# Kernel tuning notes

Measured on AMD Instinct MI355X. Metric: run time of the kernel, lower is better.

Reference implementation:

```python
import jax, jax.numpy as jnp
import numpy as np

B, N, K, IN = 8, 2048, 8, 5
BN = B * N

def _lin(k, i, o):
    s = 1.0 / np.sqrt(i)
    return jax.random.uniform(k, (i, o), jnp.float32, -s, s)

def setup_inputs() -> dict:
    key = jax.random.key(0)
    ks = jax.random.split(key, 12)
    inp = {"points": jax.random.normal(ks[0], (B, N, IN), jnp.float32)}
    dims = [(IN * 2, 64), (64 * 2, 128), (128 * 2, 256)]
    for n, (i, o) in enumerate(dims, 1):
        inp[f"W{n}"] = _lin(ks[n], i, o)
        inp[f"b{n}"] = jnp.zeros((o,), jnp.float32)
        inp[f"g{n}"] = jnp.ones((o,), jnp.float32)
        inp[f"be{n}"] = jnp.zeros((o,), jnp.float32)
    inp["Wf1"] = _lin(ks[10], 448, 512); inp["bf1"] = jnp.zeros((512,), jnp.float32)
    inp["gf"] = jnp.ones((512,), jnp.float32); inp["bef"] = jnp.zeros((512,), jnp.float32)
    inp["Wf2"] = _lin(ks[11], 512, 128); inp["bf2"] = jnp.zeros((128,), jnp.float32)
    return inp

def _lrelu(x):
    return jnp.where(x >= 0, x, 0.2 * x)

def _bn(x, g, b, eps=1e-5):
    # BatchNorm1d in training mode: per-feature batch statistics
    m = x.mean(0)
    v = x.var(0)
    return (x - m) * jax.lax.rsqrt(v + eps) * g + b

def _knn_idx(pos):
    # pos: [B,N,3] -> neighbor indices [B,N,K], self excluded
    sq = (pos * pos).sum(-1)
    d = sq[:, :, None] + sq[:, None, :] - 2.0 * jnp.einsum('bnc,bmc->bnm', pos, pos)
    d = d + jnp.eye(N, dtype=d.dtype) * 1e10  # exclude self
    _, idx = jax.lax.top_k(-d, K)
    return idx

def _edge_conv(x, src, dst, W, b, g, be):
    # PyG EdgeConv: msg = nn(cat[x_i, x_j - x_i]); aggr='max' at target i
    xc = x[dst]
    xn = x[src]
    h = jnp.concatenate([xc, xn - xc], axis=-1) @ W + b
    h = _bn(_lrelu(h), g, be)
    return jax.ops.segment_max(h, dst, num_segments=BN)

def reference(points, W1, b1, g1, be1, W2, b2, g2, be2, W3, b3, g3, be3,
              Wf1, bf1, gf, bef, Wf2, bf2):
    pos = points[..., :3]                      # [B,N,3]
    idx = _knn_idx(pos)                        # [B,N,K]
    offs = (jnp.arange(B) * N)[:, None, None]
    src = (idx + offs).reshape(-1)             # neighbor (source) node ids [E]
    dst = jnp.repeat(jnp.arange(BN), K)        # center (target) node ids [E]
    x = points.reshape(BN, IN)
    x1 = _edge_conv(x, src, dst, W1, b1, g1, be1)   # [BN,64]
    x2 = _edge_conv(x1, src, dst, W2, b2, g2, be2)  # [BN,128]
    x3 = _edge_conv(x2, src, dst, W3, b3, g3, be3)  # [BN,256]
    xs = jnp.concatenate([x1, x2, x3], axis=-1).reshape(B, N, 448)
    gfeat = xs.max(axis=1)                     # global max pool per cloud [B,448]
    h = _bn(_lrelu(gfeat @ Wf1 + bf1), gf, bef)
    return h @ Wf2 + bf2                       # [B,128]
```

## Files before the change

kernel.cpp:

```cpp
#include <hip/hip_runtime.h>
#include <math.h>

#define B_ 8
#define N_ 2048
#define K_ 8
#define IN_ 5
#define BN_ (B_*N_)
#define NEDGE_ (BN_*K_)
#define GRP 8
#define SEG_ 32
#define CSEG_ (N_/SEG_)
#define CHUNKS_ (N_/GRP)

typedef unsigned short ushort8_ __attribute__((ext_vector_type(8)));
typedef short bf16x8_ __attribute__((ext_vector_type(8)));
typedef float f32x4_ __attribute__((ext_vector_type(4)));

__device__ inline unsigned short f2bf(float f) {
    unsigned int u = __float_as_uint(f);
    u += 0x7fffu + ((u >> 16) & 1u);
    return (unsigned short)(u >> 16);
}
__device__ inline float bf2f(unsigned short h) {
    return __uint_as_float(((unsigned int)h) << 16);
}

__device__ inline unsigned int ord_f32(float f) {
    unsigned int u = __float_as_uint(f);
    return (u & 0x80000000u) ? ~u : (u | 0x80000000u);
}

__global__ __launch_bounds__(256) void knn_part(const float4* __restrict__ P4,
                                                unsigned long long* __restrict__ part) {
    int tid = threadIdx.x;
    int q = blockIdx.x * 256 + tid;
    int b = q >> 11;
    int nloc = q & (N_-1);
    int seg = blockIdx.y;

    float4 qp = P4[q];
    float qx2 = -2.0f*qp.x, qy2 = -2.0f*qp.y, qz2 = -2.0f*qp.z;
    float qsq = qp.w;

    unsigned long long best[K_];
#pragma unroll
    for (int k = 0; k < K_; ++k) best[k] = ~0ull;

    const float4* __restrict__ cb = P4 + (size_t)b*N_ + (size_t)seg*CSEG_;
    int jbase = seg * CSEG_;

#pragma unroll 4
    for (int jj = 0; jj < CSEG_; ++jj) {
        float4 c = cb[jj];
        float d = qsq + c.w;
        d = fmaf(qx2, c.x, d);
        d = fmaf(qy2, c.y, d);
        d = fmaf(qz2, c.z, d);
        int jg = jbase + jj;
        d = (jg == nloc) ? INFINITY : d;
        unsigned long long cur = ((unsigned long long)ord_f32(d) << 32) | (unsigned int)jg;
#pragma unroll
        for (int p = 0; p < K_; ++p) {
            unsigned long long lo = best[p] < cur ? best[p] : cur;
            unsigned long long hi = best[p] < cur ? cur : best[p];
            best[p] = lo; cur = hi;
        }
    }
    unsigned long long* op = part + ((size_t)seg * BN_ + q) * K_;
#pragma unroll
    for (int k = 0; k < K_; ++k) op[k] = best[k];
}

__global__ __launch_bounds__(128) void knn_merge(const unsigned long long* __restrict__ part,
                                                 int* __restrict__ src) {
    int q = blockIdx.x * 128 + threadIdx.x;
    int b = q / N_;
    unsigned long long best[K_];
#pragma unroll
    for (int k = 0; k < K_; ++k) best[k] = ~0ull;
    for (int s = 0; s < SEG_; ++s) {
        const unsigned long long* lp = part + ((size_t)s * BN_ + q) * K_;
#pragma unroll
        for (int k = 0; k < K_; ++k) {
            unsigned long long key = lp[k];
            if (key >= best[K_-1]) break;
            unsigned long long cur = key;
#pragma unroll
            for (int p = 0; p < K_; ++p) {
                unsigned long long lo = best[p] < cur ? best[p] : cur;
                unsigned long long hi = best[p] < cur ? cur : best[p];
                best[p] = lo; cur = hi;
            }
        }
    }
#pragma unroll
    for (int k = 0; k < K_; ++k)
        src[(size_t)q*K_ + k] = b*N_ + (int)(best[k] & 0xFFFFFFFFu);
}

__global__ __launch_bounds__(256) void cast_split(const float* __restrict__ X,
                                                  unsigned short* __restrict__ Xh,
                                                  unsigned short* __restrict__ Xl,
                                                  float4* __restrict__ P4,
                                                  int Kin, int Kpad, int total8) {
    int t = blockIdx.x * 256 + threadIdx.x;
    if (t < total8) {
        int vpr = Kpad >> 3;
        int m = t / vpr;
        int k0 = (t % vpr) * 8;
        ushort8_ vh, vl;
#pragma unroll
        for (int j = 0; j < 8; ++j) {
            int k = k0 + j;
            float v = (k < Kin) ? X[(size_t)m*Kin + k] : 0.0f;
            unsigned short h = f2bf(v);
            vh[j] = h;
            vl[j] = f2bf(v - bf2f(h));
        }
        *(ushort8_*)(Xh + (size_t)m*Kpad + k0) = vh;
        *(ushort8_*)(Xl + (size_t)m*Kpad + k0) = vl;
    }
    if (t < BN_) {
        const float* p = X + (size_t)t*Kin;
        float x = p[0], y = p[1], z = p[2];
        P4[t] = make_float4(x, y, z, x*x + y*y + z*z);
    }
}

__global__ __launch_bounds__(256) void prep_layer(const float* __restrict__ W,
                                                  const float* __restrict__ scale,
                                                  const float* __restrict__ shift,
                                                  const float* __restrict__ bias,
                                                  unsigned short* __restrict__ WTh,
                                                  unsigned short* __restrict__ WTl,
                                                  float* __restrict__ cvec,
                                                  int Cin, int C, int Kpad) {
    int idx = blockIdx.x * 256 + threadIdx.x;
    int nWT = 2*C*Kpad;
    if (idx < nWT) {
        int n = idx / Kpad;
        int k = idx % Kpad;
        float val = 0.0f;
        if (k < Cin) {
            float s = scale ? scale[k] : 1.0f;
            if (n < C) val = s * (W[(size_t)k*C + n] - W[(size_t)(Cin+k)*C + n]);
            else       val = s * W[(size_t)(Cin+k)*C + (n - C)];
        }
        unsigned short h = f2bf(val);
        WTh[(size_t)n*Kpad + k] = h;
        WTl[(size_t)n*Kpad + k] = f2bf(val - bf2f(h));
    } else if (idx < nWT + C) {
        int c = idx - nWT;
        float acc = bias[c];
        if (shift)
            for (int d = 0; d < Cin; ++d) acc += shift[d] * W[(size_t)d*C + c];
        cvec[c] = acc;
    }
}

__global__ __launch_bounds__(256) void mfma_dual(const unsigned short* __restrict__ Xh,
                                                 const unsigned short* __restrict__ Xl,
                                                 const unsigned short* __restrict__ WTh,
                                                 const unsigned short* __restrict__ WTl,
                                                 float* __restrict__ PQ, int K, int Ntot,
                                                 int gx) {
    __shared__ unsigned short sXh[128*32], sXl[128*32], sWh[128*32], sWl[128*32];
    int n = blockIdx.x;
    int by = (n & 7) + 8*(n/(8*gx));
    int bx = (n >> 3) % gx;
    int tid = threadIdx.x, l = tid & 63, w = tid >> 6;
    int wr = w >> 1, wc = w & 1;
    int bm = by * 128, bn0 = bx * 128;

    f32x4_ acc[4][4];
#pragma unroll
    for (int i = 0; i < 4; ++i)
#pragma unroll
        for (int j = 0; j < 4; ++j) acc[i][j] = (f32x4_){0.f, 0.f, 0.f, 0.f};

    for (int k0 = 0; k0 < K; k0 += 32) {
#pragma unroll
        for (int i = 0; i < 2; ++i) {
            int idx = tid + i*256;
            int row = idx >> 2;
            int col0 = (idx & 3) * 8;
            size_t gxo = (size_t)(bm  + row)*K + k0 + col0;
            size_t gwo = (size_t)(bn0 + row)*K + k0 + col0;
            int lo_ = ((row << 6) | (col0 << 1)) ^ ((row & 7) << 4);
            *(ushort8_*)((char*)sXh + lo_) = *(const ushort8_*)(Xh + gxo);
            *(ushort8_*)((char*)sXl + lo_) = *(const ushort8_*)(Xl + gxo);
            *(ushort8_*)((char*)sWh + lo_) = *(const ushort8_*)(WTh + gwo);
            *(ushort8_*)((char*)sWl + lo_) = *(const ushort8_*)(WTl + gwo);
        }
        __syncthreads();

        int kb = (l >> 4) << 4;
        bf16x8_ bh[4], bl4[4];
#pragma unroll
        for (int nf = 0; nf < 4; ++nf) {
            int rn = wc*64 + nf*16 + (l & 15);
            int o = ((rn << 6) | kb) ^ ((rn & 7) << 4);
            bh[nf]  = *(const bf16x8_*)((const char*)sWh + o);
            bl4[nf] = *(const bf16x8_*)((const char*)sWl + o);
        }
#pragma unroll
        for (int mf = 0; mf < 4; ++mf) {
            int rm = wr*64 + mf*16 + (l & 15);
            int o = ((rm << 6) | kb) ^ ((rm & 7) << 4);
            bf16x8_ ah = *(const bf16x8_*)((const char*)sXh + o);
            bf16x8_ al = *(const bf16x8_*)((const char*)sXl + o);
#pragma unroll
            for (int nf = 0; nf < 4; ++nf) {
                acc[mf][nf] = __builtin_amdgcn_mfma_f32_16x16x32_bf16(ah, bh[nf],  acc[mf][nf], 0, 0, 0);
                acc[mf][nf] = __builtin_amdgcn_mfma_f32_16x16x32_bf16(ah, bl4[nf], acc[mf][nf], 0, 0, 0);
                acc[mf][nf] = __builtin_amdgcn_mfma_f32_16x16x32_bf16(al, bh[nf],  acc[mf][nf], 0, 0, 0);
            }
        }
        __syncthreads();
    }

    int r0 = (l >> 4) << 2, cB = l & 15;
#pragma unroll
    for (int mf = 0; mf < 4; ++mf)
#pragma unroll
        for (int nf = 0; nf < 4; ++nf) {
            int col = bn0 + wc*64 + nf*16 + cB;
#pragma unroll
            for (int reg = 0; reg < 4; ++reg) {
                int row = bm + wr*64 + mf*16 + r0 + reg;
                PQ[(size_t)row*Ntot + col] = acc[mf][nf][reg];
            }
        }
}

__global__ void combine_kernel(const float* __restrict__ P, const float* __restrict__ Q,
                               const float* __restrict__ cvec, const int* __restrict__ src,
                               unsigned short* __restrict__ Xh_out, unsigned short* __restrict__ Xl_out,
                               float* __restrict__ partial, float* __restrict__ gpart,
                               int C, int S) {
    int pb = blockIdx.x;
    int lb = (pb & 7) * CHUNKS_ + (pb >> 3);
    int c = threadIdx.x;
    int i0 = lb * GRP;
    float cv = cvec[c];
    float sum = 0.f, ssq = 0.f;
    float bmx = -INFINITY;
    for (int g = 0; g < GRP; ++g) {
        int i = i0 + g;
        float p = P[(size_t)i*S + c] + cv;
        float mx = -INFINITY;
#pragma unroll
        for (int k = 0; k < K_; ++k) {
            int s = src[(size_t)i*K_ + k];
            float h = p + Q[(size_t)s*S + c];
            float l = (h >= 0.f) ? h : 0.2f*h;
            sum += l; ssq += l*l;
            mx = fmaxf(mx, l);
        }
        if (Xh_out) {
            unsigned short hh = f2bf(mx);
            Xh_out[(size_t)i*C + c] = hh;
            Xl_out[(size_t)i*C + c] = f2bf(mx - bf2f(hh));
        }
        bmx = fmaxf(bmx, mx);
    }
    gpart[(size_t)lb*C + c] = bmx;
    partial[(size_t)lb*2*C + c]     = sum;
    partial[(size_t)lb*2*C + C + c] = ssq;
}

__global__ __launch_bounds__(256) void reduce_kernel(const float* __restrict__ partial, int nblocks, int C,
                              const float* __restrict__ g, const float* __restrict__ be,
                              float* __restrict__ scale, float* __restrict__ shift) {
    int c = blockIdx.x;
    float s0 = 0.f, s1 = 0.f;
    for (int blk = threadIdx.x; blk < nblocks; blk += 256) {
        s0 += partial[(size_t)blk*2*C + c];
        s1 += partial[(size_t)blk*2*C + C + c];
    }
    __shared__ float l0[256], l1[256];
    l0[threadIdx.x] = s0; l1[threadIdx.x] = s1;
    __syncthreads();
    for (int off = 128; off > 0; off >>= 1) {
        if (threadIdx.x < off) {
            l0[threadIdx.x] += l0[threadIdx.x + off];
            l1[threadIdx.x] += l1[threadIdx.x + off];
        }
        __syncthreads();
    }
    if (threadIdx.x == 0) {
        float mean = l0[0] / (float)NEDGE_;
        float var  = l1[0] / (float)NEDGE_ - mean*mean;
        float sc = g[c] * rsqrtf(var + 1e-5f);
        scale[c] = sc;
        shift[c] = be[c] - mean*sc;
    }
}

__global__ __launch_bounds__(1024) void gmax_finalize(
        const float* __restrict__ gp1, const float* __restrict__ gp2, const float* __restrict__ gp3,
        const float* __restrict__ sc1, const float* __restrict__ sh1,
        const float* __restrict__ sc2, const float* __restrict__ sh2,
        const float* __restrict__ sc3, const float* __restrict__ sh3,
        float* __restrict__ gfeat) {
    int b = blockIdx.x, grp = blockIdx.y;
    const float *gp, *sc, *sh; int C, c0, coff;
    if (grp == 0)      { gp = gp1; sc = sc1; sh = sh1; C = 64;  c0 = 0;            coff = 0;   }
    else if (grp <= 2) { gp = gp2; sc = sc2; sh = sh2; C = 128; c0 = (grp-1)*64;   coff = 64;  }
    else               { gp = gp3; sc = sc3; sh = sh3; C = 256; c0 = (grp-3)*64;   coff = 192; }
    int cl = threadIdx.x & 63;
    int stripe = threadIdx.x >> 6;
    int c = c0 + cl;
    float mx = -INFINITY;
    for (int ch = stripe; ch < CHUNKS_; ch += 16)
        mx = fmaxf(mx, gp[((size_t)b*CHUNKS_ + ch)*C + c]);
    __shared__ float red[16][64];
    red[stripe][cl] = mx;
    __syncthreads();
    for (int off = 8; off > 0; off >>= 1) {
        if (stripe < off) red[stripe][cl] = fmaxf(red[stripe][cl], red[stripe+off][cl]);
        __syncthreads();
    }
    if (stripe == 0)
        gfeat[b*448 + coff + c] = sc[c]*red[0][cl] + sh[c];
}

__global__ __launch_bounds__(256) void final1(const float* __restrict__ gfeat,
                                              const float* __restrict__ Wf1, const float* __restrict__ bf1,
                                              const float* __restrict__ gf, const float* __restrict__ bef,
                                              float* __restrict__ H) {
    __shared__ float gfs[B_][448];
    __shared__ float red[4][64][B_];
    int t = threadIdx.x;
    int cl = t & 63;
    int stripe = t >> 6;
    int c = blockIdx.x * 64 + cl;
    for (int e = t; e < B_*448; e += 256) gfs[e/448][e%448] = gfeat[e];
    __syncthreads();
    float acc[B_] = {};
    for (int d = stripe*112; d < stripe*112 + 112; ++d) {
        float w = Wf1[(size_t)d*512 + c];
#pragma unroll
        for (int r = 0; r < B_; ++r) acc[r] += gfs[r][d] * w;
    }
#pragma unroll
    for (int r = 0; r < B_; ++r) red[stripe][cl][r] = acc[r];
    __syncthreads();
    if (stripe == 0) {
        float v[B_];
        float b1v = bf1[c];
#pragma unroll
        for (int r = 0; r < B_; ++r) {
            float a = red[0][cl][r] + red[1][cl][r] + red[2][cl][r] + red[3][cl][r] + b1v;
            v[r] = (a >= 0.f) ? a : 0.2f*a;
        }
        float mean = 0.f;
#pragma unroll
        for (int r = 0; r < B_; ++r) mean += v[r];
        mean *= (1.0f/B_);
        float var = 0.f;
#pragma unroll
        for (int r = 0; r < B_; ++r) { float dd = v[r] - mean; var += dd*dd; }
        var *= (1.0f/B_);
        float sc = gf[c] * rsqrtf(var + 1e-5f);
        float sh = bef[c] - mean*sc;
#pragma unroll
        for (int r = 0; r < B_; ++r) H[(size_t)r*512 + c] = v[r]*sc + sh;
    }
}

__global__ __launch_bounds__(128) void final2(const float* __restrict__ H,
                                              const float* __restrict__ Wf2, const float* __restrict__ bf2,
                                              float* __restrict__ out) {
    int b = blockIdx.x, c = threadIdx.x;
    __shared__ float hs[512];
    for (int e = c; e < 512; e += 128) hs[e] = H[(size_t)b*512 + e];
    __syncthreads();
    float a = bf2[c];
    for (int d = 0; d < 512; ++d) a += hs[d] * Wf2[(size_t)d*128 + c];
    out[b*128 + c] = a;
}

static void run_layer(int Kpad, int C,
                      const float* W, const float* g, const float* be, const float* b,
                      const float* scale_in, const float* shift_in,
                      float* PQ, const unsigned short* Xh_in, const unsigned short* Xl_in,
                      unsigned short* Xh_next, unsigned short* Xl_next,
                      unsigned short* WTh, unsigned short* WTl, float* cvec,
                      const int* src, float* partial, float* gpart,
                      float* scale_out, float* shift_out, hipStream_t stream) {
    int Cin = (scale_in == nullptr) ? IN_ : Kpad;
    int nPrep = 2*C*Kpad + C;
    int gx = 2*C/128;
    prep_layer<<<(nPrep + 255)/256, 256, 0, stream>>>(W, scale_in, shift_in, b, WTh, WTl, cvec, Cin, C, Kpad);
    mfma_dual<<<gx*(BN_/128), 256, 0, stream>>>(Xh_in, Xl_in, WTh, WTl, PQ, Kpad, 2*C, gx);
    combine_kernel<<<BN_/GRP, C, 0, stream>>>(PQ, PQ + C, cvec, src, Xh_next, Xl_next, partial, gpart, C, 2*C);
    reduce_kernel<<<C, 256, 0, stream>>>(partial, BN_/GRP, C, g, be, scale_out, shift_out);
}

extern "C" void kernel_launch(void* const* d_in, const int* in_sizes, int n_in,
                              void* d_out, int out_size, void* d_ws, size_t ws_size,
                              hipStream_t stream) {
    (void)in_sizes; (void)n_in; (void)out_size; (void)ws_size;
    const float* points = (const float*)d_in[0];
    const float* W1 = (const float*)d_in[1];  const float* b1 = (const float*)d_in[2];
    const float* g1 = (const float*)d_in[3];  const float* be1 = (const float*)d_in[4];
    const float* W2 = (const float*)d_in[5];  const float* b2 = (const float*)d_in[6];
    const float* g2 = (const float*)d_in[7];  const float* be2 = (const float*)d_in[8];
    const float* W3 = (const float*)d_in[9];  const float* b3 = (const float*)d_in[10];
    const float* g3 = (const float*)d_in[11]; const float* be3 = (const float*)d_in[12];
    const float* Wf1 = (const float*)d_in[13]; const float* bf1 = (const float*)d_in[14];
    const float* gf = (const float*)d_in[15];  const float* bef = (const float*)d_in[16];
    const float* Wf2 = (const float*)d_in[17]; const float* bf2 = (const float*)d_in[18];
    float* out = (float*)d_out;

    size_t off = 0;
    char* base = (char*)d_ws;
    auto carve = [&](size_t bytes) -> void* {
        void* p = base + off;
        off += (bytes + 255) & ~(size_t)255;
        return p;
    };
    int*   src     = (int*)  carve((size_t)NEDGE_ * 4);
    float* PQ      = (float*)carve((size_t)BN_ * 512 * 4);
    float* gp1     = (float*)carve((size_t)(BN_/GRP) * 64 * 4);
    float* gp2     = (float*)carve((size_t)(BN_/GRP) * 128 * 4);
    float* gp3     = (float*)carve((size_t)(BN_/GRP) * 256 * 4);
    unsigned short* XhA = (unsigned short*)carve((size_t)BN_ * 128 * 2);
    unsigned short* XlA = (unsigned short*)carve((size_t)BN_ * 128 * 2);
    unsigned short* XhB = (unsigned short*)carve((size_t)BN_ * 128 * 2);
    unsigned short* XlB = (unsigned short*)carve((size_t)BN_ * 128 * 2);
    unsigned short* WTh = (unsigned short*)carve((size_t)512 * 128 * 2);
    unsigned short* WTl = (unsigned short*)carve((size_t)512 * 128 * 2);
    float4* P4     = (float4*)carve((size_t)BN_ * 16);
    float* cvec    = (float*)carve(256 * 4);
    float* sc1     = (float*)carve(64 * 4);
    float* sh1     = (float*)carve(64 * 4);
    float* sc2     = (float*)carve(128 * 4);
    float* sh2     = (float*)carve(128 * 4);
    float* sc3     = (float*)carve(256 * 4);
    float* sh3     = (float*)carve(256 * 4);
    float* partial = (float*)carve((size_t)(BN_/GRP) * 2 * 256 * 4);
    float* gfeat   = (float*)carve((size_t)B_ * 448 * 4);
    float* H       = (float*)carve((size_t)B_ * 512 * 4);

    int total8 = BN_ * 32 / 8;
    cast_split<<<(total8 + 255)/256, 256, 0, stream>>>(points, XhA, XlA, P4, IN_, 32, total8);

    unsigned long long* part = (unsigned long long*)PQ;
    knn_part<<<dim3(BN_/256, SEG_), 256, 0, stream>>>(P4, part);
    knn_merge<<<BN_/128, 128, 0, stream>>>(part, src);

    run_layer(32, 64,  W1, g1, be1, b1, nullptr, nullptr,
              PQ, XhA, XlA, XhB, XlB, WTh, WTl, cvec, src, partial, gp1, sc1, sh1, stream);
    run_layer(64, 128, W2, g2, be2, b2, sc1, sh1,
              PQ, XhB, XlB, XhA, XlA, WTh, WTl, cvec, src, partial, gp2, sc2, sh2, stream);
    run_layer(128, 256, W3, g3, be3, b3, sc2, sh2,
              PQ, XhA, XlA, nullptr, nullptr, WTh, WTl, cvec, src, partial, gp3, sc3, sh3, stream);

    gmax_finalize<<<dim3(B_, 7), 1024, 0, stream>>>(gp1, gp2, gp3,
                                                    sc1, sh1, sc2, sh2, sc3, sh3, gfeat);

    final1<<<8, 256, 0, stream>>>(gfeat, Wf1, bf1, gf, bef, H);
    final2<<<8, 128, 0, stream>>>(H, Wf2, bf2, out);
}
```

Baseline: 233.1 us.

## Replace BN reduce kernels with fixed-point atomic accumulation; split kNN keys into 32-bit

The per-layer reduce_kernel launches are removed. combine_kernel now accumulates per-channel sums and sums of squares as fixed-point 64-bit integers with atomics, and downstream kernels derive the BN scale and shift from those accumulators in double. Separately, the kNN insertion sort compares 32-bit distance keys and carries indices alongside, instead of 64-bit composite compares. This drops three launches and a partial buffer, but adds atomic contention (2048 blocks per channel), a memset, redundant BN recomputation in prep_layer, and fixed-point quantisation of the statistics.

After: 322.6 us. +38.4%, slower.

```diff
diff --git a/kernel.cpp b/kernel.cpp
--- a/kernel.cpp
+++ b/kernel.cpp
@@ -11,6 +11,7 @@
 #define SEG_ 32
 #define CSEG_ (N_/SEG_)
 #define CHUNKS_ (N_/GRP)
+#define FIXS_ 1048576.0
 
 typedef unsigned short ushort8_ __attribute__((ext_vector_type(8)));
 typedef short bf16x8_ __attribute__((ext_vector_type(8)));
@@ -27,14 +28,25 @@
 
 __device__ inline unsigned int ord_f32(float f) {
     unsigned int u = __float_as_uint(f);
-    return (u & 0x80000000u) ? ~u : (u | 0x80000000u);
+    return u ^ (((unsigned int)((int)u >> 31)) | 0x80000000u);
+}
+
+__device__ inline void bn_from_acc(const unsigned long long* __restrict__ acc, int C,
+                                   const float* __restrict__ g, const float* __restrict__ be,
+                                   int k, float& sc, float& sh) {
+    double inv = 1.0 / (FIXS_ * (double)NEDGE_);
+    double mean = (double)(long long)acc[k] * inv;
+    double var  = (double)(long long)acc[C + k] * inv - mean*mean;
+    float s = g[k] * rsqrtf((float)var + 1e-5f);
+    sc = s;
+    sh = be[k] - (float)mean * s;
 }
 
 __global__ __launch_bounds__(256) void knn_part(const float4* __restrict__ P4,
                                                 unsigned long long* __restrict__ part) {
     int tid = threadIdx.x;
+    int bblk = blockIdx.x >> 3;
     int q = blockIdx.x * 256 + tid;
-    int b = q >> 11;
     int nloc = q & (N_-1);
     int seg = blockIdx.y;
 
@@ -42,11 +54,11 @@
     float qx2 = -2.0f*qp.x, qy2 = -2.0f*qp.y, qz2 = -2.0f*qp.z;
     float qsq = qp.w;
 
-    unsigned long long best[K_];
-#pragma unroll
-    for (int k = 0; k < K_; ++k) best[k] = ~0ull;
-
-    const float4* __restrict__ cb = P4 + (size_t)b*N_ + (size_t)seg*CSEG_;
+    unsigned int bd[K_], bi[K_];
+#pragma unroll
+    for (int k = 0; k < K_; ++k) { bd[k] = 0xFFFFFFFFu; bi[k] = 0xFFFFFFFFu; }
+
+    const float4* __restrict__ cb = P4 + ((size_t)bblk << 11) + (size_t)seg*CSEG_;
     int jbase = seg * CSEG_;
 
 #pragma unroll 4
@@ -58,17 +70,22 @@
         d = fmaf(qz2, c.z, d);
         int jg = jbase + jj;
         d = (jg == nloc) ? INFINITY : d;
-        unsigned long long cur = ((unsigned long long)ord_f32(d) << 32) | (unsigned int)jg;
+        unsigned int cd = ord_f32(d);
+        unsigned int ci = (unsigned int)jg;
 #pragma unroll
         for (int p = 0; p < K_; ++p) {
-            unsigned long long lo = best[p] < cur ? best[p] : cur;
-            unsigned long long hi = best[p] < cur ? cur : best[p];
-            best[p] = lo; cur = hi;
+            bool lt = cd < bd[p];
+            unsigned int nd = lt ? cd : bd[p];
+            unsigned int xd = lt ? bd[p] : cd;
+            unsigned int ni = lt ? ci : bi[p];
+            unsigned int xi = lt ? bi[p] : ci;
+            bd[p] = nd; cd = xd; bi[p] = ni; ci = xi;
         }
     }
     unsigned long long* op = part + ((size_t)seg * BN_ + q) * K_;
 #pragma unroll
-    for (int k = 0; k < K_; ++k) op[k] = best[k];
+    for (int k = 0; k < K_; ++k)
+        op[k] = ((unsigned long long)bd[k] << 32) | bi[k];
 }
 
 __global__ __launch_bounds__(128) void knn_merge(const unsigned long long* __restrict__ part,
@@ -128,8 +145,9 @@
 }
 
 __global__ __launch_bounds__(256) void prep_layer(const float* __restrict__ W,
-                                                  const float* __restrict__ scale,
-                                                  const float* __restrict__ shift,
+                                                  const unsigned long long* __restrict__ acc_prev,
+                                                  const float* __restrict__ g_prev,
+                                                  const float* __restrict__ be_prev,
                                                   const float* __restrict__ bias,
                                                   unsigned short* __restrict__ WTh,
                                                   unsigned short* __restrict__ WTl,
@@ -142,19 +160,28 @@
         int k = idx % Kpad;
         float val = 0.0f;
         if (k < Cin) {
-            float s = scale ? scale[k] : 1.0f;
+            float s = 1.0f;
+            if (acc_prev) { float sc, sh; bn_from_acc(acc_prev, Cin, g_prev, be_prev, k, sc, sh); s = sc; }
             if (n < C) val = s * (W[(size_t)k*C + n] - W[(size_t)(Cin+k)*C + n]);
             else       val = s * W[(size_t)(Cin+k)*C + (n - C)];
         }
         unsigned short h = f2bf(val);
         WTh[(size_t)n*Kpad + k] = h;
         WTl[(size_t)n*Kpad + k] = f2bf(val - bf2f(h));
-    } else if (idx < nWT + C) {
+    } else {
+        __shared__ float sh_s[256];
         int c = idx - nWT;
-        float acc = bias[c];
-        if (shift)
-            for (int d = 0; d < Cin; ++d) acc += shift[d] * W[(size_t)d*C + c];
-        cvec[c] = acc;
+        if (acc_prev && c < Cin) {
+            float sc, sh; bn_from_acc(acc_prev, Cin, g_prev, be_prev, c, sc, sh);
+            sh_s[c] = sh;
+        }
+        __syncthreads();
+        if (c < C) {
+            float a = bias[c];
+            if (acc_prev)
+                for (int d = 0; d < Cin; ++d) a += sh_s[d] * W[(size_t)d*C + c];
+            cvec[c] = a;
+        }
     }
 }
 
@@ -236,7 +263,7 @@
 __global__ void combine_kernel(const float* __restrict__ P, const float* __restrict__ Q,
                                const float* __restrict__ cvec, const int* __restrict__ src,
                                unsigned short* __restrict__ Xh_out, unsigned short* __restrict__ Xl_out,
-                               float* __restrict__ partial, float* __restrict__ gpart,
+                               unsigned long long* __restrict__ acc, float* __restrict__ gpart,
                                int C, int S) {
     int pb = blockIdx.x;
     int lb = (pb & 7) * CHUNKS_ + (pb >> 3);
@@ -265,49 +292,23 @@
         bmx = fmaxf(bmx, mx);
     }
     gpart[(size_t)lb*C + c] = bmx;
-    partial[(size_t)lb*2*C + c]     = sum;
-    partial[(size_t)lb*2*C + C + c] = ssq;
-}
-
-__global__ __launch_bounds__(256) void reduce_kernel(const float* __restrict__ partial, int nblocks, int C,
-                              const float* __restrict__ g, const float* __restrict__ be,
-                              float* __restrict__ scale, float* __restrict__ shift) {
-    int c = blockIdx.x;
-    float s0 = 0.f, s1 = 0.f;
-    for (int blk = threadIdx.x; blk < nblocks; blk += 256) {
-        s0 += partial[(size_t)blk*2*C + c];
-        s1 += partial[(size_t)blk*2*C + C + c];
-    }
-    __shared__ float l0[256], l1[256];
-    l0[threadIdx.x] = s0; l1[threadIdx.x] = s1;
-    __syncthreads();
-    for (int off = 128; off > 0; off >>= 1) {
-        if (threadIdx.x < off) {
-            l0[threadIdx.x] += l0[threadIdx.x + off];
-            l1[threadIdx.x] += l1[threadIdx.x + off];
-        }
-        __syncthreads();
-    }
-    if (threadIdx.x == 0) {
-        float mean = l0[0] / (float)NEDGE_;
-        float var  = l1[0] / (float)NEDGE_ - mean*mean;
-        float sc = g[c] * rsqrtf(var + 1e-5f);
-        scale[c] = sc;
-        shift[c] = be[c] - mean*sc;
-    }
+    long long qs = llrint((double)sum * FIXS_);
+    long long qq = llrint((double)ssq * FIXS_);
+    atomicAdd(&acc[c],     (unsigned long long)qs);
+    atomicAdd(&acc[C + c], (unsigned long long)qq);
 }
 
 __global__ __launch_bounds__(1024) void gmax_finalize(
         const float* __restrict__ gp1, const float* __restrict__ gp2, const float* __restrict__ gp3,
-        const float* __restrict__ sc1, const float* __restrict__ sh1,
-        const float* __restrict__ sc2, const float* __restrict__ sh2,
-        const float* __restrict__ sc3, const float* __restrict__ sh3,
+        const unsigned long long* __restrict__ a1, const float* __restrict__ g1, const float* __restrict__ be1,
+        const unsigned long long* __restrict__ a2, const float* __restrict__ g2, const float* __restrict__ be2,
+        const unsigned long long* __restrict__ a3, const float* __restrict__ g3, const float* __restrict__ be3,
         float* __restrict__ gfeat) {
     int b = blockIdx.x, grp = blockIdx.y;
-    const float *gp, *sc, *sh; int C, c0, coff;
-    if (grp == 0)      { gp = gp1; sc = sc1; sh = sh1; C = 64;  c0 = 0;            coff = 0;   }
-    else if (grp <= 2) { gp = gp2; sc = sc2; sh = sh2; C = 128; c0 = (grp-1)*64;   coff = 64;  }
-    else               { gp = gp3; sc = sc3; sh = sh3; C = 256; c0 = (grp-3)*64;   coff = 192; }
+    const float *gp, *g, *be; const unsigned long long* ac; int C, c0, coff;
+    if (grp == 0)      { gp = gp1; ac = a1; g = g1; be = be1; C = 64;  c0 = 0;          coff = 0;   }
+    else if (grp <= 2) { gp = gp2; ac = a2; g = g2; be = be2; C = 128; c0 = (grp-1)*64; coff = 64;  }
+    else               { gp = gp3; ac = a3; g = g3; be = be3; C = 256; c0 = (grp-3)*64; coff = 192; }
     int cl = threadIdx.x & 63;
     int stripe = threadIdx.x >> 6;
     int c = c0 + cl;
@@ -321,8 +322,10 @@
         if (stripe < off) red[stripe][cl] = fmaxf(red[stripe][cl], red[stripe+off][cl]);
         __syncthreads();
     }
-    if (stripe == 0)
-        gfeat[b*448 + coff + c] = sc[c]*red[0][cl] + sh[c];
+    if (stripe == 0) {
+        float sc, sh; bn_from_acc(ac, C, g, be, c, sc, sh);
+        gfeat[b*448 + coff + c] = sc*red[0][cl] + sh;
+    }
 }
 
 __global__ __launch_bounds__(256) void final1(const float* __restrict__ gfeat,
@@ -383,19 +386,19 @@
 
 static void run_layer(int Kpad, int C,
                       const float* W, const float* g, const float* be, const float* b,
-                      const float* scale_in, const float* shift_in,
+                      const unsigned long long* acc_prev, const float* g_prev, const float* be_prev,
                       float* PQ, const unsigned short* Xh_in, const unsigned short* Xl_in,
                       unsigned short* Xh_next, unsigned short* Xl_next,
                       unsigned short* WTh, unsigned short* WTl, float* cvec,
-                      const int* src, float* partial, float* gpart,
-                      float* scale_out, float* shift_out, hipStream_t stream) {
-    int Cin = (scale_in == nullptr) ? IN_ : Kpad;
+                      const int* src, unsigned long long* acc_out, float* gpart,
+                      hipStream_t stream) {
+    int Cin = (acc_prev == nullptr) ? IN_ : Kpad;
     int nPrep = 2*C*Kpad + C;
     int gx = 2*C/128;
-    prep_layer<<<(nPrep + 255)/256, 256, 0, stream>>>(W, scale_in, shift_in, b, WTh, WTl, cvec, Cin, C, Kpad);
+    prep_layer<<<(nPrep + 255)/256, 256, 0, stream>>>(W, acc_prev, g_prev, be_prev, b,
+                                                      WTh, WTl, cvec, Cin, C, Kpad);
     mfma_dual<<<gx*(BN_/128), 256, 0, stream>>>(Xh_in, Xl_in, WTh, WTl, PQ, Kpad, 2*C, gx);
-    combine_kernel<<<BN_/GRP, C, 0, stream>>>(PQ, PQ + C, cvec, src, Xh_next, Xl_next, partial, gpart, C, 2*C);
-    reduce_kernel<<<C, 256, 0, stream>>>(partial, BN_/GRP, C, g, be, scale_out, shift_out);
+    combine_kernel<<<BN_/GRP, C, 0, stream>>>(PQ, PQ + C, cvec, src, Xh_next, Xl_next, acc_out, gpart, C, 2*C);
 }
 
 extern "C" void kernel_launch(void* const* d_in, const int* in_sizes, int n_in,
@@ -434,15 +437,15 @@
     unsigned short* WTl = (unsigned short*)carve((size_t)512 * 128 * 2);
     float4* P4     = (float4*)carve((size_t)BN_ * 16);
     float* cvec    = (float*)carve(256 * 4);
-    float* sc1     = (float*)carve(64 * 4);
-    float* sh1     = (float*)carve(64 * 4);
-    float* sc2     = (float*)carve(128 * 4);
-    float* sh2     = (float*)carve(128 * 4);
-    float* sc3     = (float*)carve(256 * 4);
-    float* sh3     = (float*)carve(256 * 4);
-    float* partial = (float*)carve((size_t)(BN_/GRP) * 2 * 256 * 4);
+    unsigned long long* accAll = (unsigned long long*)carve(896 * 8);
     float* gfeat   = (float*)carve((size_t)B_ * 448 * 4);
     float* H       = (float*)carve((size_t)B_ * 512 * 4);
+
+    unsigned long long* acc1 = accAll;
+    unsigned long long* acc2 = accAll + 128;
+    unsigned long long* acc3 = accAll + 384;
+
+    hipMemsetAsync(accAll, 0, 896 * 8, stream);
 
     int total8 = BN_ * 32 / 8;
     cast_split<<<(total8 + 255)/256, 256, 0, stream>>>(points, XhA, XlA, P4, IN_, 32, total8);
@@ -451,15 +454,16 @@
     knn_part<<<dim3(BN_/256, SEG_), 256, 0, stream>>>(P4, part);
     knn_merge<<<BN_/128, 128, 0, stream>>>(part, src);
 
-    run_layer(32, 64,  W1, g1, be1, b1, nullptr, nullptr,
-              PQ, XhA, XlA, XhB, XlB, WTh, WTl, cvec, src, partial, gp1, sc1, sh1, stream);
-    run_layer(64, 128, W2, g2, be2, b2, sc1, sh1,
-              PQ, XhB, XlB, XhA, XlA, WTh, WTl, cvec, src, partial, gp2, sc2, sh2, stream);
-    run_layer(128, 256, W3, g3, be3, b3, sc2, sh2,
-              PQ, XhA, XlA, nullptr, nullptr, WTh, WTl, cvec, src, partial, gp3, sc3, sh3, stream);
+    run_layer(32, 64,  W1, g1, be1, b1, nullptr, nullptr, nullptr,
+              PQ, XhA, XlA, XhB, XlB, WTh, WTl, cvec, src, acc1, gp1, stream);
+    run_layer(64, 128, W2, g2, be2, b2, acc1, g1, be1,
+              PQ, XhB, XlB, XhA, XlA, WTh, WTl, cvec, src, acc2, gp2, stream);
+    run_layer(128, 256, W3, g3, be3, b3, acc2, g2, be2,
+              PQ, XhA, XlA, nullptr, nullptr, WTh, WTl, cvec, src, acc3, gp3, stream);
 
     gmax_finalize<<<dim3(B_, 7), 1024, 0, stream>>>(gp1, gp2, gp3,
-                                                    sc1, sh1, sc2, sh2, sc3, sh3, gfeat);
+                                                    acc1, g1, be1, acc2, g2, be2, acc3, g3, be3,
+                                                    gfeat);
 
     final1<<<8, 256, 0, stream>>>(gfeat, Wf1, bf1, gf, bef, H);
     final2<<<8, 128, 0, stream>>>(H, Wf2, bf2, out);
```
